# Optimization experiments

Hardware: AMD Instinct MI355X
Metric: run time of the kernel (lower is better)

Reference implementation:

```python
import jax, jax.numpy as jnp
import numpy as np

B = 512      # batch per stream
L = 600      # audio length (22 chunks of 75, step 25)
DIM = 256    # model dim
H = 8        # num heads (each head is full-width, per original code)
CH = [1, DIM // 4, DIM // 2, DIM]
KS = [26, 26, 25]
EPS = 1e-5
N_CHUNKS, CHUNK, STEP = 22, 75, 25


def setup_inputs() -> dict:
    key = jax.random.key(0)
    ks = iter(jax.random.split(key, 40))
    def rn(shape, scale=0.05):
        return jax.random.normal(next(ks), shape, jnp.float32) * scale
    inp = {}
    inp["audio_vec1"] = jax.random.normal(next(ks), (B, 1, L), jnp.float32)
    inp["audio_vec2"] = jax.random.normal(next(ks), (B, 1, L), jnp.float32)
    for i in range(3):
        inp[f"conv_w{i+1}"] = rn((CH[i + 1], CH[i], KS[i]))  # OIH, torch Conv1d layout
        inp[f"conv_b{i+1}"] = rn((CH[i + 1],))
        inp[f"bn_g{i+1}"] = jnp.ones((CH[i + 1],), jnp.float32)
        inp[f"bn_b{i+1}"] = jnp.zeros((CH[i + 1],), jnp.float32)
        inp[f"bn_m{i+1}"] = rn((CH[i + 1],))
        inp[f"bn_v{i+1}"] = jnp.ones((CH[i + 1],), jnp.float32)
    # per-head Q/K/V projections (stored [H, in, out]; torch Linear is x @ W.T + b)
    inp["Wq"] = rn((H, DIM, DIM)); inp["bq"] = rn((H, DIM))
    inp["Wk"] = rn((H, DIM, DIM)); inp["bk"] = rn((H, DIM))
    inp["Wv"] = rn((H, DIM, DIM)); inp["bv"] = rn((H, DIM))
    inp["fca_w"] = rn((H * DIM, DIM)); inp["fca_b"] = rn((DIM,))
    inp["fc_w"] = rn((DIM, DIM)); inp["fc_b"] = rn((DIM,))
    return inp


def _chunks(x):
    # x: [B, 1, L] -> [B*22, 1, 75] (batched chunks, chunk-major within each example)
    idx = jnp.arange(N_CHUNKS)[:, None] * STEP + jnp.arange(CHUNK)[None, :]  # [22, 75]
    c = x[:, :, idx]                      # [B, 1, 22, 75]
    return c.transpose(0, 2, 1, 3).reshape(-1, 1, CHUNK)


def _block(x, w, b, g, bt, m, v):
    # Conv1d (valid) + BatchNorm (eval) + Swish; dropout is identity in eval.
    y = jax.lax.conv_general_dilated(
        x, w, window_strides=(1,), padding="VALID",
        dimension_numbers=("NCH", "OIH", "NCH")) + b[None, :, None]
    scale = g * jax.lax.rsqrt(v + EPS)
    y = (y - m[None, :, None]) * scale[None, :, None] + bt[None, :, None]
    return y * jax.nn.sigmoid(y)


def _forward(audio_vec1, audio_vec2,
             conv_w1, conv_b1, bn_g1, bn_b1, bn_m1, bn_v1,
             conv_w2, conv_b2, bn_g2, bn_b2, bn_m2, bn_v2,
             conv_w3, conv_b3, bn_g3, bn_b3, bn_m3, bn_v3,
             Wq, bq, Wk, bk, Wv, bv, fca_w, fca_b, fc_w, fc_b):
    # Batch both streams and all 22 chunks through one conv stack.
    X = jnp.concatenate([_chunks(audio_vec1), _chunks(audio_vec2)], axis=0)  # [2*B*22,1,75]
    X = _block(X, conv_w1, conv_b1, bn_g1, bn_b1, bn_m1, bn_v1)  # [., 64, 50]
    X = _block(X, conv_w2, conv_b2, bn_g2, bn_b2, bn_m2, bn_v2)  # [., 128, 25]
    X = _block(X, conv_w3, conv_b3, bn_g3, bn_b3, bn_m3, bn_v3)  # [., 256, 1]
    feat = X[:, :, 0].reshape(-1, N_CHUNKS, DIM)  # [2B, 22, 256]

    # Multi-head attention: 8 independent full-width heads, no 1/sqrt(d) scaling.
    Q = jnp.einsum("bse,heo->bhso", feat, Wq) + bq[None, :, None, :]
    K = jnp.einsum("bse,heo->bhso", feat, Wk) + bk[None, :, None, :]
    V = jnp.einsum("bse,heo->bhso", feat, Wv) + bv[None, :, None, :]
    A = jax.nn.softmax(jnp.einsum("bhso,bhto->bhst", Q, K), axis=-1)
    O = jnp.einsum("bhst,bhto->bhso", A, V)          # [2B, H, 22, 256]
    O = O.transpose(0, 2, 1, 3).reshape(O.shape[0], N_CHUNKS, H * DIM)
    out = O @ fca_w + fca_b                            # [2B, 22, 256]

    pooled = out.mean(axis=1)                          # [2B, 256]
    y = pooled @ fc_w + fc_b                           # [2B, 256]
    nb = audio_vec1.shape[0]
    return y[:nb], y[nb:]


def reference(audio_vec1, audio_vec2,
              conv_w1, conv_b1, bn_g1, bn_b1, bn_m1, bn_v1,
              conv_w2, conv_b2, bn_g2, bn_b2, bn_m2, bn_v2,
              conv_w3, conv_b3, bn_g3, bn_b3, bn_m3, bn_v3,
              Wq, bq, Wk, bk, Wv, bv, fca_w, fca_b, fc_w, fc_b):
    return _forward(audio_vec1, audio_vec2,
                    conv_w1, conv_b1, bn_g1, bn_b1, bn_m1, bn_v1,
                    conv_w2, conv_b2, bn_g2, bn_b2, bn_m2, bn_v2,
                    conv_w3, conv_b3, bn_g3, bn_b3, bn_m3, bn_v3,
                    Wq, bq, Wk, bk, Wv, bv, fca_w, fca_b, fc_w, fc_b)
```

## Files before the change

kernel.cpp:

```cpp
#include <hip/hip_runtime.h>
#include <hip/hip_bf16.h>
#include <math.h>

#define NSEQ 22528
#define HALFSEQ 11264

typedef __attribute__((ext_vector_type(8))) short short8;
typedef __attribute__((ext_vector_type(4))) float f32x4;
typedef __attribute__((ext_vector_type(4))) ushort ushort4v;

__device__ __forceinline__ ushort f2bf(float x) {
    __hip_bfloat16 h = __float2bfloat16(x);
    return *reinterpret_cast<ushort*>(&h);
}
__device__ __forceinline__ float bf2f(ushort u) {
    unsigned v = ((unsigned)u) << 16;
    return *reinterpret_cast<float*>(&v);
}

__global__ __launch_bounds__(256) void k_prep_misc(
    const float* __restrict__ Wk, float* __restrict__ WkT,
    const float* __restrict__ bq, float* __restrict__ kb,
    const float* __restrict__ bv, const float* __restrict__ fca_w,
    const float* __restrict__ fca_b, float* __restrict__ bvc,
    const float* __restrict__ Wv, float* __restrict__ F)
{
    __shared__ float smem[16 * 256];
    const int bid = blockIdx.x;
    const int tid = threadIdx.x;

    if (bid < 2048) {
        int idx = bid * 256 + tid;
        int b = idx >> 16;
        int rem = idx & 65535;
        int c = rem >> 8;
        int r = rem & 255;
        WkT[idx] = Wk[(size_t)(b * 256 + r) * 256 + c];
    } else if (bid < 2056) {
        int h = bid - 2048;
        smem[tid] = bq[h * 256 + tid];
        __syncthreads();
        const float* wk = Wk + (size_t)(h * 256 + tid) * 256;
        float a = 0.f;
        for (int o = 0; o < 256; ++o) a += wk[o] * smem[o];
        kb[h * 256 + tid] = a;
    } else if (bid < 2057) {
        for (int i = tid; i < 2048; i += 256) smem[i] = bv[i];
        __syncthreads();
        float acc = fca_b[tid];
        for (int k = 0; k < 2048; ++k) acc += smem[k] * fca_w[(size_t)k * 256 + tid];
        bvc[tid] = acc;
    } else {
        int lb = bid - 2057;
        int h = lb >> 4;
        int e0 = (lb & 15) * 16;
        for (int idx = tid; idx < 4096; idx += 256) {
            int r = idx >> 8;
            int c = idx & 255;
            smem[r * 256 + c] = Wv[(size_t)h * 65536 + (e0 + r) * 256 + c];
        }
        __syncthreads();
        float acc[16];
        #pragma unroll
        for (int r = 0; r < 16; ++r) acc[r] = 0.f;
        for (int o = 0; o < 256; ++o) {
            float w = fca_w[(size_t)(h * 256 + o) * 256 + tid];
            #pragma unroll
            for (int r = 0; r < 16; ++r) acc[r] += smem[r * 256 + o] * w;
        }
        #pragma unroll
        for (int r = 0; r < 16; ++r)
            F[(size_t)(h * 256 + e0 + r) * 256 + tid] = acc[r];
    }
}

__global__ __launch_bounds__(256) void k_prep_w2t(
    const float* __restrict__ w2, ushort* __restrict__ w2f)
{
    __shared__ float tile[13312];
    const int mt = blockIdx.x >> 1;
    const int ich = blockIdx.x & 1;
    const int tid = threadIdx.x;
    for (int idx = tid; idx < 13312; idx += 256) {
        int oc16 = idx / 832;
        int rem = idx - oc16 * 832;
        tile[idx] = w2[(size_t)(mt * 16 + oc16) * 1664 + ich * 832 + rem];
    }
    __syncthreads();
    for (int wi = tid; wi < 26 * 512; wi += 256) {
        int t = wi >> 9;
        int li = wi & 511;
        int lane = li >> 3;
        int j = li & 7;
        int oc16 = lane & 15;
        int il = ((lane >> 4) << 3) + j;
        w2f[(size_t)(((2 * t + ich) * 8 + mt) << 9) + li] = f2bf(tile[oc16 * 832 + il * 26 + t]);
    }
}

__global__ __launch_bounds__(256) void k_prep_w3t(
    const float* __restrict__ w3, ushort* __restrict__ w3f)
{
    __shared__ float tile[12800];
    const int mt = blockIdx.x >> 2;
    const int icb = blockIdx.x & 3;
    const int tid = threadIdx.x;
    for (int idx = tid; idx < 12800; idx += 256) {
        int oc16 = idx / 800;
        int rem = idx - oc16 * 800;
        tile[idx] = w3[(size_t)(mt * 16 + oc16) * 3200 + icb * 800 + rem];
    }
    __syncthreads();
    for (int wi = tid; wi < 25 * 512; wi += 256) {
        int pos = wi >> 9;
        int li = wi & 511;
        int lane = li >> 3;
        int j = li & 7;
        int oc16 = lane & 15;
        int il = ((lane >> 4) << 3) + j;
        w3f[(size_t)(((pos * 4 + icb) * 16 + mt) << 9) + li] = f2bf(tile[oc16 * 800 + il * 25 + pos]);
    }
}

__global__ __launch_bounds__(256) void k_prep_attn_m(
    const float* __restrict__ Wq, const float* __restrict__ WkT,
    float* __restrict__ M)
{
    const int h = blockIdx.x >> 4;
    const int e0 = (blockIdx.x & 15) * 16;
    const int tid = threadIdx.x;
    __shared__ float sq[16][256];
    for (int idx = tid; idx < 4096; idx += 256) {
        int r = idx >> 8;
        int c = idx & 255;
        sq[r][c] = Wq[(size_t)(h * 256 + e0 + r) * 256 + c];
    }
    __syncthreads();
    float acc[16];
    #pragma unroll
    for (int r = 0; r < 16; ++r) acc[r] = 0.f;
    const float* wkt = WkT + (size_t)h * 65536 + tid;
    for (int o = 0; o < 256; ++o) {
        float wk = wkt[o * 256];
        #pragma unroll
        for (int r = 0; r < 16; ++r) acc[r] += sq[r][o] * wk;
    }
    #pragma unroll
    for (int r = 0; r < 16; ++r)
        M[(size_t)(h * 256 + e0 + r) * 256 + tid] = acc[r];
}

__global__ void k_prep_mfrag(const float* __restrict__ M, ushort* __restrict__ Mfrag,
                             const float* __restrict__ kb, ushort* __restrict__ kbf) {
    int bid = blockIdx.x;
    int tid = threadIdx.x;
    if (bid < 2048) {
        int idx = bid * 256 + tid;
        int j = idx & 7;
        int lane = (idx >> 3) & 63;
        int mt = (idx >> 9) & 15;
        int kt = (idx >> 13) & 7;
        int h = idx >> 16;
        int e = kt * 32 + ((lane >> 4) << 3) + j;
        int o = mt * 16 + (lane & 15);
        Mfrag[idx] = f2bf(M[(size_t)(h * 256 + e) * 256 + o]);
    } else {
        int idx = (bid - 2048) * 256 + tid;
        int j = idx & 7;
        int lane = (idx >> 3) & 63;
        int kt = idx >> 9;
        int h = lane & 15;
        int e = kt * 32 + ((lane >> 4) << 3) + j;
        kbf[idx] = (h < 8) ? f2bf(kb[h * 256 + e]) : (ushort)0;
    }
}

__global__ __launch_bounds__(512, 4) void k_conv(
    const float* __restrict__ av1, const float* __restrict__ av2,
    const float* __restrict__ w1,
    const float* __restrict__ b1c, const float* __restrict__ g1,
    const float* __restrict__ be1, const float* __restrict__ m1, const float* __restrict__ v1,
    const ushort* __restrict__ w2f,
    const float* __restrict__ b2c, const float* __restrict__ g2,
    const float* __restrict__ be2, const float* __restrict__ m2, const float* __restrict__ v2,
    ushort* __restrict__ a2f, int seqoff)
{
    __shared__ ushort s_a1[8 * 3200];
    __shared__ ushort s_w1f[2048];
    __shared__ ushort s_xb[8][80];
    __shared__ float s_sc1[64], s_sh1[64], s_sc2[128], s_sh2[128];

    const int tid = threadIdx.x;
    const int lane = tid & 63;
    const int w = tid >> 6;
    const int l15 = lane & 15;
    const int grp = lane >> 4;
    const int lseq0 = blockIdx.x * 8;
    const int gseq0 = seqoff + lseq0;

    for (int idx = tid; idx < 640; idx += 512) {
        int s = idx / 80;
        int i = idx - s * 80;
        int seq = gseq0 + s;
        const float* src;
        if (seq < HALFSEQ) { int b = seq / 22; int n = seq - b * 22; src = av1 + b * 600 + n * 25; }
        else { int q = seq - HALFSEQ; int b = q / 22; int n = q - b * 22; src = av2 + b * 600 + n * 25; }
        s_xb[s][i] = f2bf((i < 75) ? src[i] : 0.f);
    }
    for (int idx = tid; idx < 2048; idx += 512) {
        int j = idx & 7;
        int ln = (idx >> 3) & 63;
        int mt = idx >> 9;
        int oc = mt * 16 + (ln & 15);
        int k = ((ln >> 4) << 3) + j;
        s_w1f[idx] = (k < 26) ? f2bf(w1[oc * 26 + k]) : (ushort)0;
    }
    if (tid < 64) { float A = g1[tid] * rsqrtf(v1[tid] + 1e-5f); s_sc1[tid] = A; s_sh1[tid] = (b1c[tid] - m1[tid]) * A + be1[tid]; }
    if (tid >= 128 && tid < 256) {
        int o = tid - 128;
        float A = g2[o] * rsqrtf(v2[o] + 1e-5f); s_sc2[o] = A; s_sh2[o] = (b2c[o] - m2[o]) * A + be2[o];
    }
    __syncthreads();

    {
        short8 a1f[4];
        #pragma unroll
        for (int mt = 0; mt < 4; ++mt)
            a1f[mt] = *(const short8*)(s_w1f + mt * 512 + lane * 8);

        for (int nt = w; nt < 25; nt += 8) {
            int n = nt * 16 + l15;
            int s = n / 50;
            int p = n - s * 50;
            short8 bf;
            #pragma unroll
            for (int j = 0; j < 8; ++j) {
                int t = grp * 8 + j;
                bf[j] = (t < 26) ? (short)s_xb[s][p + t] : (short)0;
            }
            #pragma unroll
            for (int mt = 0; mt < 4; ++mt) {
                f32x4 acc1 = (f32x4){0.f, 0.f, 0.f, 0.f};
                acc1 = __builtin_amdgcn_mfma_f32_16x16x32_bf16(a1f[mt], bf, acc1, 0, 0, 0);
                int oc0 = mt * 16 + grp * 4;
                int icb = oc0 >> 3;
                int boff = s * 6400 + icb * 800 + p * 16 + (oc0 & 7) * 2;
                ushort4v u;
                #pragma unroll
                for (int r = 0; r < 4; ++r) {
                    float y = acc1[r] * s_sc1[oc0 + r] + s_sh1[oc0 + r];
                    y = y / (1.f + __expf(-y));
                    u[r] = f2bf(y);
                }
                *(ushort4v*)((char*)s_a1 + boff) = u;
            }
        }
    }
    __syncthreads();

    {
        const int mset = w & 3;
        const int nset = w >> 2;
        const int NT = nset ? 6 : 7;

        int vaddr[7];
        #pragma unroll
        for (int ni = 0; ni < 7; ++ni) {
            int nt = nset * 7 + ni;
            int n = nt * 16 + l15;
            int s = n / 25; if (s > 7) s = 7;
            int p = n - s * 25; if (p > 24) p = 24;
            vaddr[ni] = s * 6400 + grp * 800 + p * 16;
        }

        f32x4 acc[2][7];
        #pragma unroll
        for (int mi = 0; mi < 2; ++mi)
            #pragma unroll
            for (int ni = 0; ni < 7; ++ni)
                acc[mi][ni] = (f32x4){0.f, 0.f, 0.f, 0.f};

        const ushort* wpt = w2f + (size_t)(mset * 2) * 512 + lane * 8;
        short8 afA0 = *(const short8*)(wpt);
        short8 afA1 = *(const short8*)(wpt + 512);
        short8 afB0 = *(const short8*)(wpt + 4096);
        short8 afB1 = *(const short8*)(wpt + 4096 + 512);

        for (int t = 0; t < 26; ++t) {
            #pragma unroll
            for (int ni = 0; ni < 7; ++ni) {
                if (ni >= NT) break;
                short8 bf = *(const short8*)((const char*)s_a1 + vaddr[ni]);
                acc[0][ni] = __builtin_amdgcn_mfma_f32_16x16x32_bf16(afA0, bf, acc[0][ni], 0, 0, 0);
                acc[1][ni] = __builtin_amdgcn_mfma_f32_16x16x32_bf16(afA1, bf, acc[1][ni], 0, 0, 0);
            }
            if (t < 25) {
                afA0 = *(const short8*)(wpt + 8192);
                afA1 = *(const short8*)(wpt + 8192 + 512);
            }
            #pragma unroll
            for (int ni = 0; ni < 7; ++ni) {
                if (ni >= NT) break;
                short8 bf = *(const short8*)((const char*)s_a1 + vaddr[ni] + 3200);
                acc[0][ni] = __builtin_amdgcn_mfma_f32_16x16x32_bf16(afB0, bf, acc[0][ni], 0, 0, 0);
                acc[1][ni] = __builtin_amdgcn_mfma_f32_16x16x32_bf16(afB1, bf, acc[1][ni], 0, 0, 0);
            }
            if (t < 25) {
                afB0 = *(const short8*)(wpt + 12288);
                afB1 = *(const short8*)(wpt + 12288 + 512);
                wpt += 8192;
            }
            #pragma unroll
            for (int ni = 0; ni < 7; ++ni) vaddr[ni] += 16;
        }

        #pragma unroll
        for (int mi = 0; mi < 2; ++mi) {
            const int ocb = mset * 32 + mi * 16 + grp * 4;
            const int grp_dst = (ocb >> 3) & 3;
            const int jb = ocb & 7;
            const int kthi = ocb >> 5;
            #pragma unroll
            for (int ni = 0; ni < 7; ++ni) {
                if (ni >= NT) break;
                int n = (nset * 7 + ni) * 16 + l15;
                if (n < 200) {
                    int s = n / 25;
                    int p = n - s * 25;
                    int seq = lseq0 + s;
                    int kt3 = p * 4 + kthi;
                    ushort4v u;
                    #pragma unroll
                    for (int r = 0; r < 4; ++r) {
                        float y = acc[mi][ni][r] * s_sc2[ocb + r] + s_sh2[ocb + r];
                        y = y / (1.f + __expf(-y));
                        u[r] = f2bf(y);
                    }
                    *(ushort4v*)(a2f + (((size_t)(seq >> 4) * 100 + kt3) << 9)
                                 + ((seq & 15) + 16 * grp_dst) * 8 + jb) = u;
                }
            }
        }
    }
}

__global__ __launch_bounds__(256) void k_conv3(
    const ushort* __restrict__ a2f, const ushort* __restrict__ w3f,
    const float* __restrict__ b3c, const float* __restrict__ g3,
    const float* __restrict__ be3, const float* __restrict__ m3, const float* __restrict__ v3,
    float* __restrict__ feat, int seqoff)
{
    const int tid = threadIdx.x;
    const int lane = tid & 63;
    const int wv = tid >> 6;
    const int l15 = lane & 15;
    const int grp = lane >> 4;
    const int sb = blockIdx.x >> 1;
    const int mh = blockIdx.x & 1;
    const int lseq0 = sb * 64;
    const int mtb = mh * 8 + wv * 2;

    f32x4 acc3[2][4];
    #pragma unroll
    for (int mi = 0; mi < 2; ++mi)
        #pragma unroll
        for (int nt = 0; nt < 4; ++nt)
            acc3[mi][nt] = (f32x4){0.f, 0.f, 0.f, 0.f};

    const ushort* bp = a2f + ((size_t)(lseq0 >> 4) * 100) * 512 + lane * 8;
    const ushort* ap = w3f + (size_t)mtb * 512 + lane * 8;

    for (int kt = 0; kt < 100; ++kt) {
        short8 bf[4];
        #pragma unroll
        for (int nt = 0; nt < 4; ++nt)
            bf[nt] = *(const short8*)(bp + (size_t)(nt * 100 + kt) * 512);
        #pragma unroll
        for (int mi = 0; mi < 2; ++mi) {
            short8 af = *(const short8*)(ap + (size_t)kt * 8192 + mi * 512);
            #pragma unroll
            for (int nt = 0; nt < 4; ++nt)
                acc3[mi][nt] = __builtin_amdgcn_mfma_f32_16x16x32_bf16(af, bf[nt], acc3[mi][nt], 0, 0, 0);
        }
    }

    #pragma unroll
    for (int nt = 0; nt < 4; ++nt) {
        int gseq = seqoff + lseq0 + nt * 16 + l15;
        #pragma unroll
        for (int mi = 0; mi < 2; ++mi) {
            int oc = (mtb + mi) * 16 + grp * 4;
            float4 o4;
            #pragma unroll
            for (int r = 0; r < 4; ++r) {
                float A = g3[oc + r] * rsqrtf(v3[oc + r] + 1e-5f);
                float y = acc3[mi][nt][r] * A + (b3c[oc + r] - m3[oc + r]) * A + be3[oc + r];
                ((float*)&o4)[r] = y / (1.f + __expf(-y));
            }
            *(float4*)(feat + (size_t)gseq * 256 + oc) = o4;
        }
    }
}

__global__ __launch_bounds__(512, 2) void k_attn_f(
    const float* __restrict__ feat, const ushort* __restrict__ Mfrag,
    const ushort* __restrict__ kbf, float* __restrict__ fbar_all)
{
    const int g0 = blockIdx.x * 2;
    const int tid = threadIdx.x;
    const int lane = tid & 63;
    const int wv = tid >> 6;
    const int l15 = lane & 15;
    const int grp = lane >> 4;

    __shared__ __align__(16) ushort sfb[2 * 32 * 256];
    __shared__ __align__(16) ushort sG[2 * 32 * 256];
    __shared__ float sS[2 * 528];
    __shared__ float sbet[2 * 192];
    __shared__ float sab[2 * 24];

    char* const sfbb = (char*)sfb;
    char* const sGb = (char*)sG;

    for (int idx = tid; idx < 16384; idx += 512) {
        int gg = idx >> 13;
        int s = (idx >> 8) & 31;
        int e = idx & 255;
        float f = (s < 22) ? feat[(size_t)(g0 + gg) * 5632 + s * 256 + e] : 0.f;
        int byte = gg * 16384 + s * 512 + ((e * 2) ^ ((s & 7) << 4));
        *(ushort*)(sfbb + byte) = f2bf(f);
    }
    __syncthreads();

    if (wv < 4) {
        int gg = wv >> 1;
        int rowb = (wv & 1) * 16;
        int rA = rowb + l15;
        f32x4 acc = (f32x4){0.f, 0.f, 0.f, 0.f};
        for (int kt = 0; kt < 8; ++kt) {
            int e0b = (kt * 32 + grp * 8) * 2;
            short8 af = *(const short8*)(sfbb + gg * 16384 + rA * 512 + (e0b ^ ((rA & 7) << 4)));
            short8 bf = *(const short8*)(kbf + kt * 512 + lane * 8);
            acc = __builtin_amdgcn_mfma_f32_16x16x32_bf16(af, bf, acc, 0, 0, 0);
        }
        #pragma unroll
        for (int r = 0; r < 4; ++r) {
            int t = rowb + grp * 4 + r;
            int h = l15;
            if (t < 22 && h < 8) sbet[gg * 192 + h * 24 + t] = acc[r];
        }
    }
    __syncthreads();

    for (int h = 0; h < 8; ++h) {
        {
            f32x4 accg[4][2];
            #pragma unroll
            for (int mt = 0; mt < 4; ++mt)
                #pragma unroll
                for (int fi = 0; fi < 2; ++fi)
                    accg[mt][fi] = (f32x4){0.f, 0.f, 0.f, 0.f};

            const ushort* mfb = Mfrag + (size_t)h * 65536;
            for (int kt = 0; kt < 8; ++kt) {
                int e0b = (kt * 32 + grp * 8) * 2;
                short8 af[4];
                #pragma unroll
                for (int mt = 0; mt < 4; ++mt) {
                    int gg = mt >> 1;
                    int rA = (mt & 1) * 16 + l15;
                    af[mt] = *(const short8*)(sfbb + gg * 16384 + rA * 512 + (e0b ^ ((rA & 7) << 4)));
                }
                #pragma unroll
                for (int fi = 0; fi < 2; ++fi) {
                    int ft = wv * 2 + fi;
                    short8 bfm = *(const short8*)(mfb + (size_t)((kt * 16 + ft) << 9) + lane * 8);
                    #pragma unroll
                    for (int mt = 0; mt < 4; ++mt)
                        accg[mt][fi] = __builtin_amdgcn_mfma_f32_16x16x32_bf16(af[mt], bfm, accg[mt][fi], 0, 0, 0);
                }
            }
            #pragma unroll
            for (int mt = 0; mt < 4; ++mt) {
                int gg = mt >> 1;
                #pragma unroll
                for (int fi = 0; fi < 2; ++fi) {
                    int f = (wv * 2 + fi) * 16 + l15;
                    #pragma unroll
                    for (int r = 0; r < 4; ++r) {
                        int s = (mt & 1) * 16 + grp * 4 + r;
                        if (s < 22) {
                            int byte = gg * 16384 + s * 512 + ((f * 2) ^ ((s & 7) << 4));
                            *(ushort*)(sGb + byte) = f2bf(accg[mt][fi][r]);
                        }
                    }
                }
            }
        }
        __syncthreads();

        {
            int gg = wv >> 2;
            int mt2 = (wv >> 1) & 1;
            int nt2 = wv & 1;
            f32x4 sacc = (f32x4){0.f, 0.f, 0.f, 0.f};
            int sA = mt2 * 16 + l15;
            int tB = nt2 * 16 + l15;
            for (int kt = 0; kt < 8; ++kt) {
                int f0b = (kt * 32 + grp * 8) * 2;
                short8 ga = *(const short8*)(sGb + gg * 16384 + sA * 512 + (f0b ^ ((sA & 7) << 4)));
                short8 fb = *(const short8*)(sfbb + gg * 16384 + tB * 512 + (f0b ^ ((tB & 7) << 4)));
                sacc = __builtin_amdgcn_mfma_f32_16x16x32_bf16(ga, fb, sacc, 0, 0, 0);
            }
            #pragma unroll
            for (int r = 0; r < 4; ++r) {
                int s = mt2 * 16 + grp * 4 + r;
                int t = nt2 * 16 + l15;
                if (s < 22 && t < 22)
                    sS[gg * 528 + s * 24 + t] = sacc[r] + sbet[gg * 192 + h * 24 + t];
            }
        }
        __syncthreads();

        if (tid < 44) {
            int gg = tid >= 22;
            int s = tid - gg * 22;
            float* row = sS + gg * 528 + s * 24;
            float mx = -1e30f;
            #pragma unroll
            for (int t = 0; t < 22; ++t) mx = fmaxf(mx, row[t]);
            float ex[22];
            float sum = 0.f;
            #pragma unroll
            for (int t = 0; t < 22; ++t) { float e2 = __expf(row[t] - mx); ex[t] = e2; sum += e2; }
            float inv = 1.f / sum;
            #pragma unroll
            for (int t = 0; t < 22; ++t) row[t] = ex[t] * inv;
        }
        __syncthreads();
        if (tid < 44) {
            int gg = tid >= 22;
            int t = tid - gg * 22;
            float a = 0.f;
            #pragma unroll
            for (int s = 0; s < 22; ++s) a += sS[gg * 528 + s * 24 + t];
            sab[gg * 24 + t] = a * (1.f / 22.f);
        }
        __syncthreads();

        {
            int gg = tid >> 8;
            int e = tid & 255;
            int e2b = e * 2;
            float a = 0.f;
            #pragma unroll
            for (int t = 0; t < 22; ++t) {
                ushort u = *(ushort*)(sfbb + gg * 16384 + t * 512 + (e2b ^ ((t & 7) << 4)));
                a += sab[gg * 24 + t] * bf2f(u);
            }
            fbar_all[((size_t)(g0 + gg) * 8 + h) * 256 + e] = a;
        }
        __syncthreads();
    }
}

__global__ __launch_bounds__(256) void k_pool(
    const float* __restrict__ fbar_all, const float* __restrict__ F,
    const float* __restrict__ bvc,
    const float* __restrict__ fc_w, const float* __restrict__ fc_b,
    float* __restrict__ out)
{
    const int g0 = blockIdx.x * 8;
    const int tid = threadIdx.x;
    __shared__ __align__(16) float sfb[8 * 2048];
    __shared__ __align__(16) float sp[8 * 256];
    for (int idx = tid; idx < 16384; idx += 256)
        sfb[idx] = fbar_all[(size_t)g0 * 8 * 256 + idx];
    __syncthreads();

    float p[8];
    float bb = bvc[tid];
    #pragma unroll
    for (int j = 0; j < 8; ++j) p[j] = bb;
    for (int k = 0; k < 2048; k += 4) {
        float f0 = F[(size_t)(k + 0) * 256 + tid];
        float f1 = F[(size_t)(k + 1) * 256 + tid];
        float f2 = F[(size_t)(k + 2) * 256 + tid];
        float f3 = F[(size_t)(k + 3) * 256 + tid];
        #pragma unroll
        for (int j = 0; j < 8; ++j) {
            float4 v = *(const float4*)(sfb + j * 2048 + k);
            p[j] += v.x * f0 + v.y * f1 + v.z * f2 + v.w * f3;
        }
    }
    #pragma unroll
    for (int j = 0; j < 8; ++j) sp[j * 256 + tid] = p[j];
    __syncthreads();

    float y[8];
    float fb = fc_b[tid];
    #pragma unroll
    for (int j = 0; j < 8; ++j) y[j] = fb;
    for (int e = 0; e < 256; ++e) {
        float w = fc_w[(size_t)e * 256 + tid];
        #pragma unroll
        for (int j = 0; j < 8; ++j) y[j] += sp[j * 256 + e] * w;
    }
    #pragma unroll
    for (int j = 0; j < 8; ++j)
        out[(size_t)(g0 + j) * 256 + tid] = y[j];
}

extern "C" void kernel_launch(void* const* d_in, const int* in_sizes, int n_in,
                              void* d_out, int out_size, void* d_ws, size_t ws_size,
                              hipStream_t stream) {
    (void)in_sizes; (void)n_in; (void)out_size;

    const float* av1   = (const float*)d_in[0];
    const float* av2   = (const float*)d_in[1];
    const float* w1    = (const float*)d_in[2];
    const float* b1c   = (const float*)d_in[3];
    const float* g1    = (const float*)d_in[4];
    const float* be1   = (const float*)d_in[5];
    const float* m1    = (const float*)d_in[6];
    const float* v1    = (const float*)d_in[7];
    const float* w2    = (const float*)d_in[8];
    const float* b2c   = (const float*)d_in[9];
    const float* g2    = (const float*)d_in[10];
    const float* be2   = (const float*)d_in[11];
    const float* m2    = (const float*)d_in[12];
    const float* v2    = (const float*)d_in[13];
    const float* w3    = (const float*)d_in[14];
    const float* b3c   = (const float*)d_in[15];
    const float* g3    = (const float*)d_in[16];
    const float* be3   = (const float*)d_in[17];
    const float* m3    = (const float*)d_in[18];
    const float* v3    = (const float*)d_in[19];
    const float* Wq    = (const float*)d_in[20];
    const float* bq    = (const float*)d_in[21];
    const float* Wk    = (const float*)d_in[22];
    const float* bk    = (const float*)d_in[23];
    const float* Wv    = (const float*)d_in[24];
    const float* bv    = (const float*)d_in[25];
    const float* fca_w = (const float*)d_in[26];
    const float* fca_b = (const float*)d_in[27];
    const float* fc_w  = (const float*)d_in[28];
    const float* fc_b  = (const float*)d_in[29];
    (void)bk;

    float* ws = (float*)d_ws;
    float* feat = ws;
    float* Mm   = feat + 5767168;
    float* WkT  = Mm + 524288;
    float* kb   = WkT + 524288;
    float* bvc  = kb + 2048;
    float* F    = bvc + 256;
    float* fbar = F + 524288;
    ushort* w2f = (ushort*)(fbar + 2097152);
    ushort* w3f = w2f + 212992;
    ushort* mfr = w3f + 819200;
    ushort* kbf = mfr + 524288;
    ushort* region = kbf + 4096;

    size_t base_bytes = (size_t)((char*)region - (char*)d_ws);
    size_t budget = (ws_size > base_bytes + 4096) ? (ws_size - base_bytes - 4096) : 0;
    int ncA = 16;
    const int cand[5] = {1, 2, 4, 8, 16};
    for (int i = 0; i < 5; ++i) { if ((size_t)144179200 / cand[i] <= budget) { ncA = cand[i]; break; } }
    const int seqsA = NSEQ / ncA;

    k_prep_misc<<<2185, 256, 0, stream>>>(Wk, WkT, bq, kb, bv, fca_w, fca_b, bvc, Wv, F);
    k_prep_w2t<<<16, 256, 0, stream>>>(w2, w2f);
    k_prep_w3t<<<64, 256, 0, stream>>>(w3, w3f);
    k_prep_attn_m<<<128, 256, 0, stream>>>(Wq, WkT, Mm);
    k_prep_mfrag<<<2064, 256, 0, stream>>>(Mm, mfr, kb, kbf);

    ushort* a2f = region;
    for (int c = 0; c < ncA; ++c) {
        int seqoff = c * seqsA;
        k_conv<<<seqsA / 8, 512, 0, stream>>>(av1, av2,
            w1, b1c, g1, be1, m1, v1,
            w2f, b2c, g2, be2, m2, v2,
            a2f, seqoff);
        k_conv3<<<(seqsA / 64) * 2, 256, 0, stream>>>(a2f, w3f,
            b3c, g3, be3, m3, v3, feat, seqoff);
    }

    k_attn_f<<<512, 512, 0, stream>>>(feat, mfr, kbf, fbar);
    k_pool<<<128, 256, 0, stream>>>(fbar, F, bvc, fc_w, fc_b, (float*)d_out);
}
```

Measured before the change: 581.2 us.

## Fold BN scale into conv weights, widen conv3 tiles, cheaper SiLU, more pool blocks

Folds the batch-norm scale into the bf16 conv weights for all three conv layers, leaving only an additive shift in each epilogue. The SiLU now uses a hardware reciprocal, and pairs of outputs are packed to bf16 with a single instruction. conv3 drops the split over output-channel halves so each wave computes 4x4 MFMA tiles and reuses the B fragments more, at the cost of half as many blocks and more registers. k_pool processes 4 sequences per block instead of 8, doubling its block count, and the conv3 shift is precomputed in the prep kernel.

Result: faster. 555.6 us (-4.4%).

```diff
diff --git a/kernel.cpp b/kernel.cpp
--- a/kernel.cpp
+++ b/kernel.cpp
@@ -16,6 +16,15 @@
 __device__ __forceinline__ float bf2f(ushort u) {
     unsigned v = ((unsigned)u) << 16;
     return *reinterpret_cast<float*>(&v);
+}
+__device__ __forceinline__ unsigned pkbf(float lo, float hi) {
+    unsigned r;
+    asm("v_cvt_pk_bf16_f32 %0, %1, %2" : "=v"(r) : "v"(lo), "v"(hi));
+    return r;
+}
+__device__ __forceinline__ float fsilu(float y) {
+    float e = __expf(-y);
+    return y * __builtin_amdgcn_rcpf(1.f + e);
 }
 
 __global__ __launch_bounds__(256) void k_prep_misc(
@@ -23,7 +32,10 @@
     const float* __restrict__ bq, float* __restrict__ kb,
     const float* __restrict__ bv, const float* __restrict__ fca_w,
     const float* __restrict__ fca_b, float* __restrict__ bvc,
-    const float* __restrict__ Wv, float* __restrict__ F)
+    const float* __restrict__ Wv, float* __restrict__ F,
+    const float* __restrict__ b3c, const float* __restrict__ g3,
+    const float* __restrict__ be3, const float* __restrict__ m3,
+    const float* __restrict__ v3, float* __restrict__ sh3)
 {
     __shared__ float smem[16 * 256];
     const int bid = blockIdx.x;
@@ -50,7 +62,7 @@
         float acc = fca_b[tid];
         for (int k = 0; k < 2048; ++k) acc += smem[k] * fca_w[(size_t)k * 256 + tid];
         bvc[tid] = acc;
-    } else {
+    } else if (bid < 2185) {
         int lb = bid - 2057;
         int h = lb >> 4;
         int e0 = (lb & 15) * 16;
@@ -71,11 +83,15 @@
         #pragma unroll
         for (int r = 0; r < 16; ++r)
             F[(size_t)(h * 256 + e0 + r) * 256 + tid] = acc[r];
+    } else {
+        float A = g3[tid] * rsqrtf(v3[tid] + 1e-5f);
+        sh3[tid] = (b3c[tid] - m3[tid]) * A + be3[tid];
     }
 }
 
 __global__ __launch_bounds__(256) void k_prep_w2t(
-    const float* __restrict__ w2, ushort* __restrict__ w2f)
+    const float* __restrict__ w2, ushort* __restrict__ w2f,
+    const float* __restrict__ g2, const float* __restrict__ v2)
 {
     __shared__ float tile[13312];
     const int mt = blockIdx.x >> 1;
@@ -94,12 +110,15 @@
         int j = li & 7;
         int oc16 = lane & 15;
         int il = ((lane >> 4) << 3) + j;
-        w2f[(size_t)(((2 * t + ich) * 8 + mt) << 9) + li] = f2bf(tile[oc16 * 832 + il * 26 + t]);
+        int oc = mt * 16 + oc16;
+        float A = g2[oc] * rsqrtf(v2[oc] + 1e-5f);
+        w2f[(size_t)(((2 * t + ich) * 8 + mt) << 9) + li] = f2bf(tile[oc16 * 832 + il * 26 + t] * A);
     }
 }
 
 __global__ __launch_bounds__(256) void k_prep_w3t(
-    const float* __restrict__ w3, ushort* __restrict__ w3f)
+    const float* __restrict__ w3, ushort* __restrict__ w3f,
+    const float* __restrict__ g3, const float* __restrict__ v3)
 {
     __shared__ float tile[12800];
     const int mt = blockIdx.x >> 2;
@@ -118,7 +137,9 @@
         int j = li & 7;
         int oc16 = lane & 15;
         int il = ((lane >> 4) << 3) + j;
-        w3f[(size_t)(((pos * 4 + icb) * 16 + mt) << 9) + li] = f2bf(tile[oc16 * 800 + il * 25 + pos]);
+        int oc = mt * 16 + oc16;
+        float A = g3[oc] * rsqrtf(v3[oc] + 1e-5f);
+        w3f[(size_t)(((pos * 4 + icb) * 16 + mt) << 9) + li] = f2bf(tile[oc16 * 800 + il * 25 + pos] * A);
     }
 }
 
@@ -188,7 +209,7 @@
     __shared__ ushort s_a1[8 * 3200];
     __shared__ ushort s_w1f[2048];
     __shared__ ushort s_xb[8][80];
-    __shared__ float s_sc1[64], s_sh1[64], s_sc2[128], s_sh2[128];
+    __shared__ float s_sh1[64], s_sh2[128];
 
     const int tid = threadIdx.x;
     const int lane = tid & 63;
@@ -213,12 +234,17 @@
         int mt = idx >> 9;
         int oc = mt * 16 + (ln & 15);
         int k = ((ln >> 4) << 3) + j;
-        s_w1f[idx] = (k < 26) ? f2bf(w1[oc * 26 + k]) : (ushort)0;
-    }
-    if (tid < 64) { float A = g1[tid] * rsqrtf(v1[tid] + 1e-5f); s_sc1[tid] = A; s_sh1[tid] = (b1c[tid] - m1[tid]) * A + be1[tid]; }
+        float A = g1[oc] * rsqrtf(v1[oc] + 1e-5f);
+        s_w1f[idx] = (k < 26) ? f2bf(w1[oc * 26 + k] * A) : (ushort)0;
+    }
+    if (tid < 64) {
+        float A = g1[tid] * rsqrtf(v1[tid] + 1e-5f);
+        s_sh1[tid] = (b1c[tid] - m1[tid]) * A + be1[tid];
+    }
     if (tid >= 128 && tid < 256) {
         int o = tid - 128;
-        float A = g2[o] * rsqrtf(v2[o] + 1e-5f); s_sc2[o] = A; s_sh2[o] = (b2c[o] - m2[o]) * A + be2[o];
+        float A = g2[o] * rsqrtf(v2[o] + 1e-5f);
+        s_sh2[o] = (b2c[o] - m2[o]) * A + be2[o];
     }
     __syncthreads();
 
@@ -245,14 +271,14 @@
                 int oc0 = mt * 16 + grp * 4;
                 int icb = oc0 >> 3;
                 int boff = s * 6400 + icb * 800 + p * 16 + (oc0 & 7) * 2;
-                ushort4v u;
-                #pragma unroll
-                for (int r = 0; r < 4; ++r) {
-                    float y = acc1[r] * s_sc1[oc0 + r] + s_sh1[oc0 + r];
-                    y = y / (1.f + __expf(-y));
-                    u[r] = f2bf(y);
-                }
-                *(ushort4v*)((char*)s_a1 + boff) = u;
+                float y0 = fsilu(acc1[0] + s_sh1[oc0 + 0]);
+                float y1 = fsilu(acc1[1] + s_sh1[oc0 + 1]);
+                float y2 = fsilu(acc1[2] + s_sh1[oc0 + 2]);
+                float y3 = fsilu(acc1[3] + s_sh1[oc0 + 3]);
+                uint2 u;
+                u.x = pkbf(y0, y1);
+                u.y = pkbf(y2, y3);
+                *(uint2*)((char*)s_a1 + boff) = u;
             }
         }
     }
@@ -329,15 +355,15 @@
                     int p = n - s * 25;
                     int seq = lseq0 + s;
                     int kt3 = p * 4 + kthi;
-                    ushort4v u;
-                    #pragma unroll
-                    for (int r = 0; r < 4; ++r) {
-                        float y = acc[mi][ni][r] * s_sc2[ocb + r] + s_sh2[ocb + r];
-                        y = y / (1.f + __expf(-y));
-                        u[r] = f2bf(y);
-                    }
-                    *(ushort4v*)(a2f + (((size_t)(seq >> 4) * 100 + kt3) << 9)
-                                 + ((seq & 15) + 16 * grp_dst) * 8 + jb) = u;
+                    float y0 = fsilu(acc[mi][ni][0] + s_sh2[ocb + 0]);
+                    float y1 = fsilu(acc[mi][ni][1] + s_sh2[ocb + 1]);
+                    float y2 = fsilu(acc[mi][ni][2] + s_sh2[ocb + 2]);
+                    float y3 = fsilu(acc[mi][ni][3] + s_sh2[ocb + 3]);
+                    uint2 u;
+                    u.x = pkbf(y0, y1);
+                    u.y = pkbf(y2, y3);
+                    *(uint2*)(a2f + (((size_t)(seq >> 4) * 100 + kt3) << 9)
+                              + ((seq & 15) + 16 * grp_dst) * 8 + jb) = u;
                 }
             }
         }
@@ -346,8 +372,7 @@
 
 __global__ __launch_bounds__(256) void k_conv3(
     const ushort* __restrict__ a2f, const ushort* __restrict__ w3f,
-    const float* __restrict__ b3c, const float* __restrict__ g3,
-    const float* __restrict__ be3, const float* __restrict__ m3, const float* __restrict__ v3,
+    const float* __restrict__ sh3,
     float* __restrict__ feat, int seqoff)
 {
     const int tid = threadIdx.x;
@@ -355,20 +380,17 @@
     const int wv = tid >> 6;
     const int l15 = lane & 15;
     const int grp = lane >> 4;
-    const int sb = blockIdx.x >> 1;
-    const int mh = blockIdx.x & 1;
-    const int lseq0 = sb * 64;
-    const int mtb = mh * 8 + wv * 2;
-
-    f32x4 acc3[2][4];
+    const int lseq0 = blockIdx.x * 64;
+
+    f32x4 acc3[4][4];
     #pragma unroll
-    for (int mi = 0; mi < 2; ++mi)
+    for (int mi = 0; mi < 4; ++mi)
         #pragma unroll
         for (int nt = 0; nt < 4; ++nt)
             acc3[mi][nt] = (f32x4){0.f, 0.f, 0.f, 0.f};
 
     const ushort* bp = a2f + ((size_t)(lseq0 >> 4) * 100) * 512 + lane * 8;
-    const ushort* ap = w3f + (size_t)mtb * 512 + lane * 8;
+    const ushort* ap = w3f + (size_t)(wv * 4) * 512 + lane * 8;
 
     for (int kt = 0; kt < 100; ++kt) {
         short8 bf[4];
@@ -376,7 +398,7 @@
         for (int nt = 0; nt < 4; ++nt)
             bf[nt] = *(const short8*)(bp + (size_t)(nt * 100 + kt) * 512);
         #pragma unroll
-        for (int mi = 0; mi < 2; ++mi) {
+        for (int mi = 0; mi < 4; ++mi) {
             short8 af = *(const short8*)(ap + (size_t)kt * 8192 + mi * 512);
             #pragma unroll
             for (int nt = 0; nt < 4; ++nt)
@@ -388,15 +410,12 @@
     for (int nt = 0; nt < 4; ++nt) {
         int gseq = seqoff + lseq0 + nt * 16 + l15;
         #pragma unroll
-        for (int mi = 0; mi < 2; ++mi) {
-            int oc = (mtb + mi) * 16 + grp * 4;
+        for (int mi = 0; mi < 4; ++mi) {
+            int oc = wv * 64 + mi * 16 + grp * 4;
             float4 o4;
             #pragma unroll
-            for (int r = 0; r < 4; ++r) {
-                float A = g3[oc + r] * rsqrtf(v3[oc + r] + 1e-5f);
-                float y = acc3[mi][nt][r] * A + (b3c[oc + r] - m3[oc + r]) * A + be3[oc + r];
-                ((float*)&o4)[r] = y / (1.f + __expf(-y));
-            }
+            for (int r = 0; r < 4; ++r)
+                ((float*)&o4)[r] = fsilu(acc3[mi][nt][r] + sh3[oc + r]);
             *(float4*)(feat + (size_t)gseq * 256 + oc) = o4;
         }
     }
@@ -570,44 +589,44 @@
     const float* __restrict__ fc_w, const float* __restrict__ fc_b,
     float* __restrict__ out)
 {
-    const int g0 = blockIdx.x * 8;
+    const int g0 = blockIdx.x * 4;
     const int tid = threadIdx.x;
-    __shared__ __align__(16) float sfb[8 * 2048];
-    __shared__ __align__(16) float sp[8 * 256];
-    for (int idx = tid; idx < 16384; idx += 256)
+    __shared__ __align__(16) float sfb[4 * 2048];
+    __shared__ __align__(16) float sp[4 * 256];
+    for (int idx = tid; idx < 8192; idx += 256)
         sfb[idx] = fbar_all[(size_t)g0 * 8 * 256 + idx];
     __syncthreads();
 
-    float p[8];
+    float p[4];
     float bb = bvc[tid];
     #pragma unroll
-    for (int j = 0; j < 8; ++j) p[j] = bb;
+    for (int j = 0; j < 4; ++j) p[j] = bb;
     for (int k = 0; k < 2048; k += 4) {
         float f0 = F[(size_t)(k + 0) * 256 + tid];
         float f1 = F[(size_t)(k + 1) * 256 + tid];
         float f2 = F[(size_t)(k + 2) * 256 + tid];
         float f3 = F[(size_t)(k + 3) * 256 + tid];
         #pragma unroll
-        for (int j = 0; j < 8; ++j) {
+        for (int j = 0; j < 4; ++j) {
             float4 v = *(const float4*)(sfb + j * 2048 + k);
             p[j] += v.x * f0 + v.y * f1 + v.z * f2 + v.w * f3;
         }
     }
     #pragma unroll
-    for (int j = 0; j < 8; ++j) sp[j * 256 + tid] = p[j];
-    __syncthreads();
-
-    float y[8];
+    for (int j = 0; j < 4; ++j) sp[j * 256 + tid] = p[j];
+    __syncthreads();
+
+    float y[4];
     float fb = fc_b[tid];
     #pragma unroll
-    for (int j = 0; j < 8; ++j) y[j] = fb;
+    for (int j = 0; j < 4; ++j) y[j] = fb;
     for (int e = 0; e < 256; ++e) {
         float w = fc_w[(size_t)e * 256 + tid];
         #pragma unroll
-        for (int j = 0; j < 8; ++j) y[j] += sp[j * 256 + e] * w;
+        for (int j = 0; j < 4; ++j) y[j] += sp[j * 256 + e] * w;
     }
     #pragma unroll
-    for (int j = 0; j < 8; ++j)
+    for (int j = 0; j < 4; ++j)
         out[(size_t)(g0 + j) * 256 + tid] = y[j];
 }
 
@@ -656,7 +675,8 @@
     float* bvc  = kb + 2048;
     float* F    = bvc + 256;
     float* fbar = F + 524288;
-    ushort* w2f = (ushort*)(fbar + 2097152);
+    float* sh3  = fbar + 2097152;
+    ushort* w2f = (ushort*)(sh3 + 256);
     ushort* w3f = w2f + 212992;
     ushort* mfr = w3f + 819200;
     ushort* kbf = mfr + 524288;
@@ -669,9 +689,10 @@
     for (int i = 0; i < 5; ++i) { if ((size_t)144179200 / cand[i] <= budget) { ncA = cand[i]; break; } }
     const int seqsA = NSEQ / ncA;
 
-    k_prep_misc<<<2185, 256, 0, stream>>>(Wk, WkT, bq, kb, bv, fca_w, fca_b, bvc, Wv, F);
-    k_prep_w2t<<<16, 256, 0, stream>>>(w2, w2f);
-    k_prep_w3t<<<64, 256, 0, stream>>>(w3, w3f);
+    k_prep_misc<<<2186, 256, 0, stream>>>(Wk, WkT, bq, kb, bv, fca_w, fca_b, bvc, Wv, F,
+                                          b3c, g3, be3, m3, v3, sh3);
+    k_prep_w2t<<<16, 256, 0, stream>>>(w2, w2f, g2, v2);
+    k_prep_w3t<<<64, 256, 0, stream>>>(w3, w3f, g3, v3);
     k_prep_attn_m<<<128, 256, 0, stream>>>(Wq, WkT, Mm);
     k_prep_mfrag<<<2064, 256, 0, stream>>>(Mm, mfr, kb, kbf);
 
@@ -682,10 +703,9 @@
             w1, b1c, g1, be1, m1, v1,
             w2f, b2c, g2, be2, m2, v2,
             a2f, seqoff);
-        k_conv3<<<(seqsA / 64) * 2, 256, 0, stream>>>(a2f, w3f,
-            b3c, g3, be3, m3, v3, feat, seqoff);
+        k_conv3<<<seqsA / 64, 256, 0, stream>>>(a2f, w3f, sh3, feat, seqoff);
     }
 
     k_attn_f<<<512, 512, 0, stream>>>(feat, mfr, kbf, fbar);
-    k_pool<<<128, 256, 0, stream>>>(fbar, F, bvc, fc_w, fc_b, (float*)d_out);
-}
+    k_pool<<<256, 256, 0, stream>>>(fbar, F, bvc, fc_w, fc_b, (float*)d_out);
+}
```
